# Kernel optimization log

Measured on AMD Instinct MI355X. Metric: run time of the kernel, lower is better.

The kernel has to match this reference:

```python
import jax, jax.numpy as jnp
import numpy as np

N = 100000      # nodes
R = 4           # relations
E = 500000      # edges per relation
IN, HID, OUT = 128, 128, 64


def _rel_conv(x, src, dst, W, b):
    """One DGL GraphConv (norm='both') over one relation's edge list.
    out = D_dst^{-1/2} * segsum_dst( D_src^{-1/2} x[src] ) @ W + b
    """
    ones = jnp.ones(src.shape[0], dtype=x.dtype)
    out_deg = jax.ops.segment_sum(ones, src, num_segments=N)
    in_deg = jax.ops.segment_sum(ones, dst, num_segments=N)
    norm_src = jax.lax.rsqrt(jnp.maximum(out_deg, 1.0))
    norm_dst = jax.lax.rsqrt(jnp.maximum(in_deg, 1.0))
    msg = (x * norm_src[:, None])[src]                       # [E, d] gather
    agg = jax.ops.segment_sum(msg, dst, num_segments=N)      # [N, d] scatter-add
    agg = agg * norm_dst[:, None]
    return agg @ W + b


def setup_inputs() -> dict:
    key = jax.random.key(0)
    ks = jax.random.split(key, 8)
    x = jax.random.normal(ks[0], (N, IN), dtype=jnp.float32)
    edge_src = jax.random.randint(ks[1], (R, E), 0, N, dtype=jnp.int32)
    edge_dst = jax.random.randint(ks[2], (R, E), 0, N, dtype=jnp.int32)
    s1 = 1.0 / np.sqrt(IN)
    s2 = 1.0 / np.sqrt(HID)
    W1 = jax.random.normal(ks[3], (R, IN, HID), dtype=jnp.float32) * s1
    b1 = jnp.zeros((R, HID), dtype=jnp.float32)
    W2 = jax.random.normal(ks[4], (R, HID, OUT), dtype=jnp.float32) * s2
    b2 = jnp.zeros((R, OUT), dtype=jnp.float32)
    return {"x": x, "edge_src": edge_src, "edge_dst": edge_dst,
            "W1": W1, "b1": b1, "W2": W2, "b2": b2}


def reference(x, edge_src, edge_dst, W1, b1, W2, b2):
    # layer 1: per-relation GraphConv, aggregate='sum' across relations
    h = _rel_conv(x, edge_src[0], edge_dst[0], W1[0], b1[0])
    for r in range(1, R):
        h = h + _rel_conv(x, edge_src[r], edge_dst[r], W1[r], b1[r])
    h = jax.nn.relu(h)
    # layer 2
    out = _rel_conv(h, edge_src[0], edge_dst[0], W2[0], b2[0])
    for r in range(1, R):
        out = out + _rel_conv(h, edge_src[r], edge_dst[r], W2[r], b2[r])
    return out
```

## Files before the change

kernel.cpp:

```cpp
#include <hip/hip_runtime.h>


constexpr int Nn  = 100000;
constexpr int Rr  = 4;
constexpr int Ee  = 500000;
constexpr int RE  = Rr * Ee;
constexpr int TOT = Rr * Nn;
constexpr int NP  = 100096;
constexpr int NPB = NP / 128;
constexpr int NB1 = 1024;
constexpr int CH  = (TOT + NB1 - 1) / NB1;

constexpr int CB2   = (RE / 2 + 255) / 256;
constexpr int GB1   = 4 * NPB;
constexpr int PAIR1 = 2 * GB1;
constexpr int P1_GRID = PAIR1 + (CB2 - GB1) + 1;

constexpr int FB = (RE / 4 + 255) / 256;

typedef short bf16x8 __attribute__((ext_vector_type(8)));
typedef float f32x4  __attribute__((ext_vector_type(4)));

__device__ __forceinline__ unsigned short f2bf(float f) {
    unsigned u = __builtin_bit_cast(unsigned, f);
    u = u + 0x7FFFu + ((u >> 16) & 1u);
    return (unsigned short)(u >> 16);
}
__device__ __forceinline__ float bf2f(unsigned short h) {
    unsigned u = ((unsigned)h) << 16;
    return __builtin_bit_cast(float, u);
}
__device__ __forceinline__ float bfbits_lo(unsigned p) {
    return __builtin_bit_cast(float, p << 16);
}
__device__ __forceinline__ float bfbits_hi(unsigned p) {
    return __builtin_bit_cast(float, p & 0xFFFF0000u);
}

__device__ __forceinline__ void count_body2(int sub, int tid,
    const int* __restrict__ src, const int* __restrict__ dst,
    unsigned* __restrict__ deg, unsigned* __restrict__ slot)
{
    int e0 = (sub * 256 + tid) * 2;
    if (e0 >= RE) return;
    int r = (unsigned)e0 / (unsigned)Ee;
    int base = r * Nn;
    int2 s2 = *reinterpret_cast<const int2*>(src + e0);
    int2 d2 = *reinterpret_cast<const int2*>(dst + e0);
    atomicAdd(&deg[base + s2.x], 1u);
    atomicAdd(&deg[base + s2.y], 1u);
    uint2 sl;
    sl.x = atomicAdd(&deg[TOT + d2.x * Rr + r], 1u);
    sl.y = atomicAdd(&deg[TOT + d2.y * Rr + r], 1u);
    *reinterpret_cast<uint2*>(slot + e0) = sl;
}

__device__ __forceinline__ void bsum_body(int tid,
    const float* __restrict__ b1, const float* __restrict__ b2,
    float* __restrict__ bs1, float* __restrict__ bs2)
{
    if (tid < 128) bs1[tid] = b1[tid] + b1[128 + tid] + b1[256 + tid] + b1[384 + tid];
    if (tid < 64)  bs2[tid] = b2[tid] + b2[64 + tid] + b2[128 + tid] + b2[192 + tid];
}

template<int BN, bool CONVA>
__device__ __forceinline__ void gemm_body(
    const short* __restrict__ Xh, const short* __restrict__ Xl,
    const float* __restrict__ Xf,
    const short* __restrict__ WhT_, const short* __restrict__ WlT_,
    short* __restrict__ Y_, int CW, int rowblk, int rel)
{
    constexpr int BM = 128, BKp = 40;
    constexpr int MFR = (BN == 128) ? 4 : 2;
    constexpr int NFR = 4;
    const short* WhT = WhT_ + (size_t)rel * (BN * 128);
    const short* WlT = WlT_ + (size_t)rel * (BN * 128);
    short* Y = Y_ + (size_t)rel * BN;

    __shared__ __align__(16) short Ah[BM * BKp], Al[BM * BKp];
    __shared__ __align__(16) short Bh[BN * BKp], Bl[BN * BKp];

    const int tid = threadIdx.x;
    const int lane = tid & 63, wid = tid >> 6;
    const int lr = lane & 15, lg = lane >> 4;
    const int wm0 = (BN == 128) ? (wid >> 1) * 64 : wid * 32;
    const int wn0 = (BN == 128) ? (wid & 1) * 64 : 0;
    const int row0 = rowblk * BM;

    f32x4 acc[MFR][NFR];
    #pragma unroll
    for (int m = 0; m < MFR; ++m)
        #pragma unroll
        for (int n = 0; n < NFR; ++n)
            #pragma unroll
            for (int j = 0; j < 4; ++j) acc[m][n][j] = 0.f;

    const int sr = tid >> 1;
    const int sko = (tid & 1) * 16;

    for (int ks = 0; ks < 4; ++ks) {
        if constexpr (CONVA) {
            int grow = row0 + sr;
            float v[16];
            if (grow < Nn) {
                const float* xp = Xf + (size_t)grow * 128 + ks * 32 + sko;
                float4 a0 = *reinterpret_cast<const float4*>(xp);
                float4 a1 = *reinterpret_cast<const float4*>(xp + 4);
                float4 a2 = *reinterpret_cast<const float4*>(xp + 8);
                float4 a3 = *reinterpret_cast<const float4*>(xp + 12);
                v[0]=a0.x; v[1]=a0.y; v[2]=a0.z; v[3]=a0.w;
                v[4]=a1.x; v[5]=a1.y; v[6]=a1.z; v[7]=a1.w;
                v[8]=a2.x; v[9]=a2.y; v[10]=a2.z; v[11]=a2.w;
                v[12]=a3.x; v[13]=a3.y; v[14]=a3.z; v[15]=a3.w;
            } else {
                #pragma unroll
                for (int i = 0; i < 16; ++i) v[i] = 0.f;
            }
            bf16x8 h0, h1, l0, l1;
            #pragma unroll
            for (int i = 0; i < 8; ++i) {
                unsigned short h = f2bf(v[i]);
                h0[i] = (short)h; l0[i] = (short)f2bf(v[i] - bf2f(h));
                unsigned short g = f2bf(v[8 + i]);
                h1[i] = (short)g; l1[i] = (short)f2bf(v[8 + i] - bf2f(g));
            }
            *reinterpret_cast<bf16x8*>(&Ah[sr * BKp + sko])     = h0;
            *reinterpret_cast<bf16x8*>(&Ah[sr * BKp + sko + 8]) = h1;
            *reinterpret_cast<bf16x8*>(&Al[sr * BKp + sko])     = l0;
            *reinterpret_cast<bf16x8*>(&Al[sr * BKp + sko + 8]) = l1;
        } else {
            size_t ga = (size_t)(row0 + sr) * 128 + ks * 32 + sko;
            *reinterpret_cast<bf16x8*>(&Ah[sr * BKp + sko])     = *reinterpret_cast<const bf16x8*>(&Xh[ga]);
            *reinterpret_cast<bf16x8*>(&Ah[sr * BKp + sko + 8]) = *reinterpret_cast<const bf16x8*>(&Xh[ga + 8]);
            *reinterpret_cast<bf16x8*>(&Al[sr * BKp + sko])     = *reinterpret_cast<const bf16x8*>(&Xl[ga]);
            *reinterpret_cast<bf16x8*>(&Al[sr * BKp + sko + 8]) = *reinterpret_cast<const bf16x8*>(&Xl[ga + 8]);
        }
        if (BN == 128 || tid < 128) {
            size_t gb = (size_t)sr * 128 + ks * 32 + sko;
            *reinterpret_cast<bf16x8*>(&Bh[sr * BKp + sko])     = *reinterpret_cast<const bf16x8*>(&WhT[gb]);
            *reinterpret_cast<bf16x8*>(&Bh[sr * BKp + sko + 8]) = *reinterpret_cast<const bf16x8*>(&WhT[gb + 8]);
            *reinterpret_cast<bf16x8*>(&Bl[sr * BKp + sko])     = *reinterpret_cast<const bf16x8*>(&WlT[gb]);
            *reinterpret_cast<bf16x8*>(&Bl[sr * BKp + sko + 8]) = *reinterpret_cast<const bf16x8*>(&WlT[gb + 8]);
        }
        __syncthreads();

        bf16x8 bh[NFR], bl[NFR];
        #pragma unroll
        for (int n = 0; n < NFR; ++n) {
            bh[n] = *reinterpret_cast<const bf16x8*>(&Bh[(wn0 + n * 16 + lr) * BKp + lg * 8]);
            bl[n] = *reinterpret_cast<const bf16x8*>(&Bl[(wn0 + n * 16 + lr) * BKp + lg * 8]);
        }
        __builtin_amdgcn_s_setprio(1);
        #pragma unroll
        for (int m = 0; m < MFR; ++m) {
            bf16x8 ah = *reinterpret_cast<const bf16x8*>(&Ah[(wm0 + m * 16 + lr) * BKp + lg * 8]);
            bf16x8 al = *reinterpret_cast<const bf16x8*>(&Al[(wm0 + m * 16 + lr) * BKp + lg * 8]);
            #pragma unroll
            for (int n = 0; n < NFR; ++n) {
                acc[m][n] = __builtin_amdgcn_mfma_f32_16x16x32_bf16(ah, bh[n], acc[m][n], 0, 0, 0);
                acc[m][n] = __builtin_amdgcn_mfma_f32_16x16x32_bf16(ah, bl[n], acc[m][n], 0, 0, 0);
                acc[m][n] = __builtin_amdgcn_mfma_f32_16x16x32_bf16(al, bh[n], acc[m][n], 0, 0, 0);
            }
        }
        __builtin_amdgcn_s_setprio(0);
        __syncthreads();
    }

    #pragma unroll
    for (int m = 0; m < MFR; ++m)
        #pragma unroll
        for (int n = 0; n < NFR; ++n) {
            int col = wn0 + n * 16 + lr;
            int rb = row0 + wm0 + m * 16 + lg * 4;
            #pragma unroll
            for (int j = 0; j < 4; ++j)
                Y[(size_t)(rb + j) * CW + col] = (short)f2bf(acc[m][n][j]);
        }
}

__global__ __launch_bounds__(256)
void phase1_kernel(const int* __restrict__ src, const int* __restrict__ dst,
                   unsigned* __restrict__ deg, unsigned* __restrict__ slot,
                   const float* __restrict__ X,
                   const short* __restrict__ w1h, const short* __restrict__ w1l,
                   short* __restrict__ Y,
                   const float* __restrict__ b1, const float* __restrict__ b2,
                   float* __restrict__ bs1, float* __restrict__ bs2)
{
    int bid = blockIdx.x, tid = threadIdx.x;
    if (bid < PAIR1) {
        int sub = bid >> 1;
        if (bid & 1) {
            int rel = sub & 3, rowblk = sub >> 2;
            gemm_body<128, true>(nullptr, nullptr, X, w1h, w1l, Y, 512, rowblk, rel);
        } else {
            count_body2(sub, tid, src, dst, deg, slot);
        }
    } else {
        int t = bid - PAIR1;
        if (t < CB2 - GB1) count_body2(GB1 + t, tid, src, dst, deg, slot);
        else              bsum_body(tid, b1, b2, bs1, bs2);
    }
}

__global__ __launch_bounds__(256)
void count_kernel(const int* __restrict__ src, const int* __restrict__ dst,
                  unsigned* __restrict__ deg, unsigned* __restrict__ slot)
{
    count_body2(blockIdx.x, threadIdx.x, src, dst, deg, slot);
}

__global__ void bsum_kernel(const float* __restrict__ b1, const float* __restrict__ b2,
                            float* __restrict__ bs1, float* __restrict__ bs2)
{
    bsum_body(threadIdx.x, b1, b2, bs1, bs2);
}

__global__ __launch_bounds__(256)
void norms_scan1_kernel(const unsigned* __restrict__ deg, float* __restrict__ nrm,
                        uint2* __restrict__ rpnd, unsigned* __restrict__ partial)
{
    __shared__ unsigned s[256];
    int b = blockIdx.x, t = threadIdx.x;
    int start = b * CH;
    int n = TOT - start; if (n > CH) n = CH;
    unsigned sum = 0;
    for (int i = t; i < n; i += 256) {
        unsigned sd = deg[start + i];
        unsigned dd = deg[TOT + start + i];
        nrm[start + i] = rsqrtf((float)(sd > 0u ? sd : 1u));
        rpnd[start + i].y = __builtin_bit_cast(unsigned, rsqrtf((float)(dd > 0u ? dd : 1u)));
        sum += dd;
    }
    s[t] = sum; __syncthreads();
    for (int d = 128; d > 0; d >>= 1) {
        if (t < d) s[t] += s[t + d];
        __syncthreads();
    }
    if (t == 0) partial[b] = s[0];
}

__global__ __launch_bounds__(1024)
void scan2_kernel(unsigned* __restrict__ partial, unsigned* __restrict__ rowptr)
{
    __shared__ unsigned s[NB1];
    int t = threadIdx.x;
    unsigned orig = partial[t];
    s[t] = orig; __syncthreads();
    for (int d = 1; d < NB1; d <<= 1) {
        unsigned v = (t >= d) ? s[t - d] : 0u;
        __syncthreads();
        s[t] += v;
        __syncthreads();
    }
    partial[t] = s[t] - orig;
    if (t == 0) rowptr[TOT] = (unsigned)RE;
}

__global__ __launch_bounds__(256)
void scan3_kernel(const unsigned* __restrict__ deg, const unsigned* __restrict__ base,
                  unsigned* __restrict__ rowptr, uint2* __restrict__ rpnd)
{
    __shared__ unsigned s[CH];
    int b = blockIdx.x, t = threadIdx.x;
    int start = b * CH;
    int n = TOT - start; if (n > CH) n = CH;
    if (n <= 0) return;
    for (int i = t; i < n; i += 256) s[i] = deg[TOT + start + i];
    __syncthreads();
    if (t == 0) {
        unsigned run = base[b];
        for (int i = 0; i < n; ++i) { unsigned v = s[i]; s[i] = run; run += v; }
    }
    __syncthreads();
    for (int i = t; i < n; i += 256) {
        unsigned v = s[i];
        rowptr[start + i] = v;
        rpnd[start + i].x = v;
    }
}

__global__ __launch_bounds__(256)
void fill_csr_kernel(const int* __restrict__ src, const int* __restrict__ dst,
                     const unsigned* __restrict__ slot, const uint2* __restrict__ rpnd,
                     const float* __restrict__ nrm, int2* __restrict__ csrw)
{
    int e0 = (blockIdx.x * 256 + threadIdx.x) * 4;
    if (e0 >= RE) return;
    int r = (unsigned)e0 / (unsigned)Ee;
    int base = r * Nn;
    int4 s4 = *reinterpret_cast<const int4*>(src + e0);
    int4 d4 = *reinterpret_cast<const int4*>(dst + e0);
    uint4 sl = *reinterpret_cast<const uint4*>(slot + e0);
    #pragma unroll
    for (int i = 0; i < 4; ++i) {
        int s = (i == 0) ? s4.x : (i == 1) ? s4.y : (i == 2) ? s4.z : s4.w;
        int d = (i == 0) ? d4.x : (i == 1) ? d4.y : (i == 2) ? d4.z : d4.w;
        unsigned k = (i == 0) ? sl.x : (i == 1) ? sl.y : (i == 2) ? sl.z : sl.w;
        uint2 rn = rpnd[d * Rr + r];
        float w = nrm[base + s] * __builtin_bit_cast(float, rn.y);
        int2 v; v.x = s | (r << 17); v.y = __builtin_bit_cast(int, w);
        csrw[rn.x + k] = v;
    }
}

__global__ __launch_bounds__(256)
void convw_kernel(const float* __restrict__ W1, const float* __restrict__ W2,
                  short* __restrict__ w1h, short* __restrict__ w1l,
                  short* __restrict__ w2h, short* __restrict__ w2l)
{
    int gid = blockIdx.x * 256 + threadIdx.x;
    if (gid < 4 * 128 * 128) {
        int r = gid >> 14, rem = gid & 16383, n = rem >> 7, k = rem & 127;
        float v = W1[(r << 14) + k * 128 + n];
        unsigned short h = f2bf(v);
        unsigned short l = f2bf(v - bf2f(h));
        w1h[(r << 14) + n * 128 + k] = (short)h;
        w1l[(r << 14) + n * 128 + k] = (short)l;
    } else {
        int g2 = gid - 65536;
        if (g2 >= 4 * 64 * 128) return;
        int r = g2 >> 13, rem = g2 & 8191, n = rem >> 7, k = rem & 127;
        float v = W2[(r << 13) + k * 64 + n];
        unsigned short h = f2bf(v);
        unsigned short l = f2bf(v - bf2f(h));
        w2h[(r << 13) + n * 128 + k] = (short)h;
        w2l[(r << 13) + n * 128 + k] = (short)l;
    }
}

template<int BN, bool CONVA>
__global__ __launch_bounds__(256)
void gemm_kernel(const short* __restrict__ Xh, const short* __restrict__ Xl,
                 const float* __restrict__ Xf,
                 const short* __restrict__ WhT_, const short* __restrict__ WlT_,
                 short* __restrict__ Y_, int CW)
{
    gemm_body<BN, CONVA>(Xh, Xl, Xf, WhT_, WlT_, Y_, CW, blockIdx.x, blockIdx.y);
}

template<int F, int NRl>
__global__ __launch_bounds__(256)
void gather_kernel(const short* __restrict__ Y, const unsigned* __restrict__ rowptr,
                   const int2* __restrict__ csrw, const float* __restrict__ bsum,
                   float* __restrict__ H, short* __restrict__ Xh, short* __restrict__ Xl,
                   int CW, int rel, int accumulate, int finalize)
{
    constexpr int FL = F / 16;
    int wid = (blockIdx.x * 256 + threadIdx.x) >> 6;
    int lane = threadIdx.x & 63;
    int q = lane >> 4, li = lane & 15;
    if (wid >= Nn) return;

    unsigned e, e1;
    if (NRl == 4) { e = rowptr[wid * 4];       e1 = rowptr[wid * 4 + 4]; }
    else          { e = rowptr[wid * 4 + rel]; e1 = rowptr[wid * 4 + rel + 1]; }

    float t[FL];
    #pragma unroll
    for (int f = 0; f < FL; ++f) t[f] = 0.f;

    auto yaddr = [&](int2 a) -> const short* {
        int s = a.x & 0x1FFFF;
        int rl = (NRl == 4) ? (a.x >> 17) : 0;
        return Y + (size_t)s * CW + rl * F + li * FL;
    };

    for (; e + 8 <= e1; e += 8) {
        int2 a = csrw[e + q], b = csrw[e + 4 + q];
        const short* ya = yaddr(a);
        const short* yb = yaddr(b);
        float wa = __builtin_bit_cast(float, a.y);
        float wb = __builtin_bit_cast(float, b.y);
        if constexpr (FL == 8) {
            uint4 pa = *reinterpret_cast<const uint4*>(ya);
            uint4 pb = *reinterpret_cast<const uint4*>(yb);
            t[0] += wa * bfbits_lo(pa.x) + wb * bfbits_lo(pb.x);
            t[1] += wa * bfbits_hi(pa.x) + wb * bfbits_hi(pb.x);
            t[2] += wa * bfbits_lo(pa.y) + wb * bfbits_lo(pb.y);
            t[3] += wa * bfbits_hi(pa.y) + wb * bfbits_hi(pb.y);
            t[4] += wa * bfbits_lo(pa.z) + wb * bfbits_lo(pb.z);
            t[5] += wa * bfbits_hi(pa.z) + wb * bfbits_hi(pb.z);
            t[6] += wa * bfbits_lo(pa.w) + wb * bfbits_lo(pb.w);
            t[7] += wa * bfbits_hi(pa.w) + wb * bfbits_hi(pb.w);
        } else {
            uint2 pa = *reinterpret_cast<const uint2*>(ya);
            uint2 pb = *reinterpret_cast<const uint2*>(yb);
            t[0] += wa * bfbits_lo(pa.x) + wb * bfbits_lo(pb.x);
            t[1] += wa * bfbits_hi(pa.x) + wb * bfbits_hi(pb.x);
            t[2] += wa * bfbits_lo(pa.y) + wb * bfbits_lo(pb.y);
            t[3] += wa * bfbits_hi(pa.y) + wb * bfbits_hi(pb.y);
        }
    }
    if (e + 4 <= e1) {
        int2 a = csrw[e + q];
        const short* ya = yaddr(a);
        float wa = __builtin_bit_cast(float, a.y);
        if constexpr (FL == 8) {
            uint4 pa = *reinterpret_cast<const uint4*>(ya);
            t[0] += wa * bfbits_lo(pa.x); t[1] += wa * bfbits_hi(pa.x);
            t[2] += wa * bfbits_lo(pa.y); t[3] += wa * bfbits_hi(pa.y);
            t[4] += wa * bfbits_lo(pa.z); t[5] += wa * bfbits_hi(pa.z);
            t[6] += wa * bfbits_lo(pa.w); t[7] += wa * bfbits_hi(pa.w);
        } else {
            uint2 pa = *reinterpret_cast<const uint2*>(ya);
            t[0] += wa * bfbits_lo(pa.x); t[1] += wa * bfbits_hi(pa.x);
            t[2] += wa * bfbits_lo(pa.y); t[3] += wa * bfbits_hi(pa.y);
        }
        e += 4;
    }
    int nrem = (int)(e1 - e);
    if (q < nrem) {
        int2 a = csrw[e + q];
        const short* ya = yaddr(a);
        float wa = __builtin_bit_cast(float, a.y);
        if constexpr (FL == 8) {
            uint4 pa = *reinterpret_cast<const uint4*>(ya);
            t[0] += wa * bfbits_lo(pa.x); t[1] += wa * bfbits_hi(pa.x);
            t[2] += wa * bfbits_lo(pa.y); t[3] += wa * bfbits_hi(pa.y);
            t[4] += wa * bfbits_lo(pa.z); t[5] += wa * bfbits_hi(pa.z);
            t[6] += wa * bfbits_lo(pa.w); t[7] += wa * bfbits_hi(pa.w);
        } else {
            uint2 pa = *reinterpret_cast<const uint2*>(ya);
            t[0] += wa * bfbits_lo(pa.x); t[1] += wa * bfbits_hi(pa.x);
            t[2] += wa * bfbits_lo(pa.y); t[3] += wa * bfbits_hi(pa.y);
        }
    }

    #pragma unroll
    for (int f = 0; f < FL; ++f) {
        t[f] += __shfl_xor(t[f], 16, 64);
        t[f] += __shfl_xor(t[f], 32, 64);
    }
    if (q != 0) return;

    float* hp = H + (size_t)wid * F + li * FL;
    if (accumulate) {
        #pragma unroll
        for (int f = 0; f < FL; ++f) t[f] += hp[f];
    } else {
        #pragma unroll
        for (int f = 0; f < FL; ++f) t[f] += bsum[li * FL + f];
    }
    if (F == 128 && finalize) {
        short hv[8], lv[8];
        #pragma unroll
        for (int f = 0; f < FL; ++f) {
            float v = fmaxf(t[f], 0.f);
            unsigned short hb = f2bf(v);
            hv[f] = (short)hb;
            lv[f] = (short)f2bf(v - bf2f(hb));
        }
        *reinterpret_cast<uint4*>(Xh + (size_t)wid * F + li * FL) = *reinterpret_cast<uint4*>(hv);
        *reinterpret_cast<uint4*>(Xl + (size_t)wid * F + li * FL) = *reinterpret_cast<uint4*>(lv);
    } else {
        if constexpr (FL == 8) {
            *reinterpret_cast<float4*>(hp)     = make_float4(t[0], t[1], t[2], t[3]);
            *reinterpret_cast<float4*>(hp + 4) = make_float4(t[4], t[5], t[6], t[7]);
        } else {
            *reinterpret_cast<float4*>(hp) = make_float4(t[0], t[1], t[2], t[3]);
        }
    }
}

extern "C" void kernel_launch(void* const* d_in, const int* in_sizes, int n_in,
                              void* d_out, int out_size, void* d_ws, size_t ws_size,
                              hipStream_t stream)
{
    const float* x  = (const float*)d_in[0];
    const int* esrc = (const int*)d_in[1];
    const int* edst = (const int*)d_in[2];
    const float* W1 = (const float*)d_in[3];
    const float* b1 = (const float*)d_in[4];
    const float* W2 = (const float*)d_in[5];
    const float* b2 = (const float*)d_in[6];
    float* out = (float*)d_out;

    char* ws = (char*)d_ws;
    size_t off = 0;
    auto alloc = [&](size_t bytes) { char* p = ws + off; off += (bytes + 255) & ~(size_t)255; return p; };
    unsigned* deg     = (unsigned*)alloc((size_t)2 * TOT * 4);
    float*    nrm     = (float*)   alloc((size_t)TOT * 4);
    uint2*    rpnd    = (uint2*)   alloc((size_t)TOT * 8);
    unsigned* rowptr  = (unsigned*)alloc((size_t)(TOT + 1) * 4);
    unsigned* partial = (unsigned*)alloc((size_t)NB1 * 4);
    unsigned* slot    = (unsigned*)alloc((size_t)RE * 4);
    float*    bs1     = (float*)   alloc(128 * 4);
    float*    bs2     = (float*)   alloc(64 * 4);
    short*    w1h     = (short*)   alloc((size_t)4 * 128 * 128 * 2);
    short*    w1l     = (short*)   alloc((size_t)4 * 128 * 128 * 2);
    short*    w2h     = (short*)   alloc((size_t)4 * 64 * 128 * 2);
    short*    w2l     = (short*)   alloc((size_t)4 * 64 * 128 * 2);
    int2*     csrw    = (int2*)    alloc((size_t)RE * 8);
    short*    xh      = (short*)   alloc((size_t)NP * 128 * 2);
    short*    xl      = (short*)   alloc((size_t)NP * 128 * 2);

    size_t yslot = (size_t)NP * 128 * 2;
    bool pathA = (ws_size >= off + 4 * yslot + 4096);
    float* h = nullptr;
    short* Y;
    if (pathA) {
        Y = (short*)alloc(4 * yslot);
    } else {
        h = (float*)alloc((size_t)NP * 128 * 4);
        Y = (short*)alloc(yslot);
    }

    const int ggrid = (Nn * 64 + 255) / 256;

    convw_kernel<<<384, 256, 0, stream>>>(W1, W2, w1h, w1l, w2h, w2l);
    hipMemsetAsync(deg, 0, (size_t)2 * TOT * 4, stream);

    if (pathA) {
        phase1_kernel<<<P1_GRID, 256, 0, stream>>>(
            esrc, edst, deg, slot, x, w1h, w1l, Y, b1, b2, bs1, bs2);
        norms_scan1_kernel<<<NB1, 256, 0, stream>>>(deg, nrm, rpnd, partial);
        scan2_kernel<<<1, NB1, 0, stream>>>(partial, rowptr);
        scan3_kernel<<<NB1, 256, 0, stream>>>(deg, partial, rowptr, rpnd);
        fill_csr_kernel<<<FB, 256, 0, stream>>>(esrc, edst, slot, rpnd, nrm, csrw);
        gather_kernel<128, 4><<<ggrid, 256, 0, stream>>>(
            Y, rowptr, csrw, bs1, (float*)out , xh, xl, 512, 0, 0, 1);
        gemm_kernel<64, false><<<dim3(NPB, 4), 256, 0, stream>>>(
            xh, xl, nullptr, w2h, w2l, Y, 256);
        gather_kernel<64, 4><<<ggrid, 256, 0, stream>>>(
            Y, rowptr, csrw, bs2, out, nullptr, nullptr, 256, 0, 0, 0);
    } else {
        count_kernel<<<CB2, 256, 0, stream>>>(esrc, edst, deg, slot);
        bsum_kernel<<<1, 128, 0, stream>>>(b1, b2, bs1, bs2);
        norms_scan1_kernel<<<NB1, 256, 0, stream>>>(deg, nrm, rpnd, partial);
        scan2_kernel<<<1, NB1, 0, stream>>>(partial, rowptr);
        scan3_kernel<<<NB1, 256, 0, stream>>>(deg, partial, rowptr, rpnd);
        fill_csr_kernel<<<FB, 256, 0, stream>>>(esrc, edst, slot, rpnd, nrm, csrw);
        for (int r = 0; r < Rr; ++r) {
            gemm_kernel<128, true><<<dim3(NPB, 1), 256, 0, stream>>>(
                nullptr, nullptr, x, w1h + (size_t)r * 128 * 128, w1l + (size_t)r * 128 * 128, Y, 128);
            gather_kernel<128, 1><<<ggrid, 256, 0, stream>>>(
                Y, rowptr, csrw, bs1, h, xh, xl, 128, r, r > 0, r == Rr - 1);
        }
        for (int r = 0; r < Rr; ++r) {
            gemm_kernel<64, false><<<dim3(NPB, 1), 256, 0, stream>>>(
                xh, xl, nullptr, w2h + (size_t)r * 64 * 128, w2l + (size_t)r * 64 * 128, Y, 64);
            gather_kernel<64, 1><<<ggrid, 256, 0, stream>>>(
                Y, rowptr, csrw, bs2, out, nullptr, nullptr, 64, r, r > 0, 0);
        }
    }
}
```

Baseline: 433.9 us.

## Fuse layer-2 GEMM across relations and widen gather unrolling

Adds a 512-thread GEMM kernel that computes all four relations' layer-2 projections in one block per 128-row tile. The A tile is loaded into shared memory once and reused across relations, instead of being reloaded by a separate grid dimension per relation. The gather kernel now unrolls four edges per quarter-wave. For F=64 it uses 8 lanes per edge with 16-byte loads instead of 16 lanes with 8-byte loads, so more edges are in flight per wave. The cost is a longer shuffle reduction and more registers and shared memory per block.

Result: faster. 396.6 us (-8.6%).

```diff
diff --git a/kernel.cpp b/kernel.cpp
--- a/kernel.cpp
+++ b/kernel.cpp
@@ -339,6 +339,77 @@
     gemm_body<BN, CONVA>(Xh, Xl, Xf, WhT_, WlT_, Y_, CW, blockIdx.x, blockIdx.y);
 }
 
+__global__ __launch_bounds__(512)
+void gemm64f_kernel(const short* __restrict__ Xh, const short* __restrict__ Xl,
+                    const short* __restrict__ w2h, const short* __restrict__ w2l,
+                    short* __restrict__ Y)
+{
+    constexpr int BKp = 40;
+    __shared__ __align__(16) short Ah[128 * BKp], Al[128 * BKp];
+    __shared__ __align__(16) short Bh[256 * BKp], Bl[256 * BKp];
+
+    const int tid = threadIdx.x;
+    const int lane = tid & 63, wv = tid >> 6;
+    const int rel = wv >> 1, wm0 = (wv & 1) * 64;
+    const int lr = lane & 15, lg = lane >> 4;
+    const int row0 = blockIdx.x * 128;
+
+    f32x4 acc[4][4];
+    #pragma unroll
+    for (int m = 0; m < 4; ++m)
+        #pragma unroll
+        for (int n = 0; n < 4; ++n)
+            #pragma unroll
+            for (int j = 0; j < 4; ++j) acc[m][n][j] = 0.f;
+
+    const int sra = tid >> 2, ska = (tid & 3) * 8;
+    const int rb = tid >> 7, nb = (tid >> 1) & 63, skb = (tid & 1) * 16;
+
+    for (int ks = 0; ks < 4; ++ks) {
+        size_t ga = (size_t)(row0 + sra) * 128 + ks * 32 + ska;
+        *reinterpret_cast<bf16x8*>(&Ah[sra * BKp + ska]) = *reinterpret_cast<const bf16x8*>(&Xh[ga]);
+        *reinterpret_cast<bf16x8*>(&Al[sra * BKp + ska]) = *reinterpret_cast<const bf16x8*>(&Xl[ga]);
+        size_t gb = (size_t)rb * (64 * 128) + (size_t)nb * 128 + ks * 32 + skb;
+        *reinterpret_cast<bf16x8*>(&Bh[(rb * 64 + nb) * BKp + skb])     = *reinterpret_cast<const bf16x8*>(&w2h[gb]);
+        *reinterpret_cast<bf16x8*>(&Bh[(rb * 64 + nb) * BKp + skb + 8]) = *reinterpret_cast<const bf16x8*>(&w2h[gb + 8]);
+        *reinterpret_cast<bf16x8*>(&Bl[(rb * 64 + nb) * BKp + skb])     = *reinterpret_cast<const bf16x8*>(&w2l[gb]);
+        *reinterpret_cast<bf16x8*>(&Bl[(rb * 64 + nb) * BKp + skb + 8]) = *reinterpret_cast<const bf16x8*>(&w2l[gb + 8]);
+        __syncthreads();
+
+        bf16x8 bh[4], bl[4];
+        #pragma unroll
+        for (int n = 0; n < 4; ++n) {
+            bh[n] = *reinterpret_cast<const bf16x8*>(&Bh[(rel * 64 + n * 16 + lr) * BKp + lg * 8]);
+            bl[n] = *reinterpret_cast<const bf16x8*>(&Bl[(rel * 64 + n * 16 + lr) * BKp + lg * 8]);
+        }
+        __builtin_amdgcn_s_setprio(1);
+        #pragma unroll
+        for (int m = 0; m < 4; ++m) {
+            bf16x8 ah = *reinterpret_cast<const bf16x8*>(&Ah[(wm0 + m * 16 + lr) * BKp + lg * 8]);
+            bf16x8 al = *reinterpret_cast<const bf16x8*>(&Al[(wm0 + m * 16 + lr) * BKp + lg * 8]);
+            #pragma unroll
+            for (int n = 0; n < 4; ++n) {
+                acc[m][n] = __builtin_amdgcn_mfma_f32_16x16x32_bf16(ah, bh[n], acc[m][n], 0, 0, 0);
+                acc[m][n] = __builtin_amdgcn_mfma_f32_16x16x32_bf16(ah, bl[n], acc[m][n], 0, 0, 0);
+                acc[m][n] = __builtin_amdgcn_mfma_f32_16x16x32_bf16(al, bh[n], acc[m][n], 0, 0, 0);
+            }
+        }
+        __builtin_amdgcn_s_setprio(0);
+        __syncthreads();
+    }
+
+    #pragma unroll
+    for (int m = 0; m < 4; ++m)
+        #pragma unroll
+        for (int n = 0; n < 4; ++n) {
+            int col = rel * 64 + n * 16 + lr;
+            int rbse = row0 + wm0 + m * 16 + lg * 4;
+            #pragma unroll
+            for (int j = 0; j < 4; ++j)
+                Y[(size_t)(rbse + j) * 256 + col] = (short)f2bf(acc[m][n][j]);
+        }
+}
+
 template<int F, int NRl>
 __global__ __launch_bounds__(256)
 void gather_kernel(const short* __restrict__ Y, const unsigned* __restrict__ rowptr,
@@ -346,10 +417,12 @@
                    float* __restrict__ H, short* __restrict__ Xh, short* __restrict__ Xl,
                    int CW, int rel, int accumulate, int finalize)
 {
-    constexpr int FL = F / 16;
+    constexpr int LPE = (F == 128) ? 16 : 8;
+    constexpr int QN  = 64 / LPE;
+    constexpr int FL  = F / LPE;
     int wid = (blockIdx.x * 256 + threadIdx.x) >> 6;
     int lane = threadIdx.x & 63;
-    int q = lane >> 4, li = lane & 15;
+    int q = lane / LPE, li = lane & (LPE - 1);
     if (wid >= Nn) return;
 
     unsigned e, e1;
@@ -365,72 +438,64 @@
         int rl = (NRl == 4) ? (a.x >> 17) : 0;
         return Y + (size_t)s * CW + rl * F + li * FL;
     };
-
-    for (; e + 8 <= e1; e += 8) {
-        int2 a = csrw[e + q], b = csrw[e + 4 + q];
-        const short* ya = yaddr(a);
-        const short* yb = yaddr(b);
-        float wa = __builtin_bit_cast(float, a.y);
-        float wb = __builtin_bit_cast(float, b.y);
-        if constexpr (FL == 8) {
-            uint4 pa = *reinterpret_cast<const uint4*>(ya);
-            uint4 pb = *reinterpret_cast<const uint4*>(yb);
-            t[0] += wa * bfbits_lo(pa.x) + wb * bfbits_lo(pb.x);
-            t[1] += wa * bfbits_hi(pa.x) + wb * bfbits_hi(pb.x);
-            t[2] += wa * bfbits_lo(pa.y) + wb * bfbits_lo(pb.y);
-            t[3] += wa * bfbits_hi(pa.y) + wb * bfbits_hi(pb.y);
-            t[4] += wa * bfbits_lo(pa.z) + wb * bfbits_lo(pb.z);
-            t[5] += wa * bfbits_hi(pa.z) + wb * bfbits_hi(pb.z);
-            t[6] += wa * bfbits_lo(pa.w) + wb * bfbits_lo(pb.w);
-            t[7] += wa * bfbits_hi(pa.w) + wb * bfbits_hi(pb.w);
-        } else {
-            uint2 pa = *reinterpret_cast<const uint2*>(ya);
-            uint2 pb = *reinterpret_cast<const uint2*>(yb);
-            t[0] += wa * bfbits_lo(pa.x) + wb * bfbits_lo(pb.x);
-            t[1] += wa * bfbits_hi(pa.x) + wb * bfbits_hi(pb.x);
-            t[2] += wa * bfbits_lo(pa.y) + wb * bfbits_lo(pb.y);
-            t[3] += wa * bfbits_hi(pa.y) + wb * bfbits_hi(pb.y);
-        }
-    }
-    if (e + 4 <= e1) {
-        int2 a = csrw[e + q];
+    auto accum1 = [&](int2 a) {
         const short* ya = yaddr(a);
         float wa = __builtin_bit_cast(float, a.y);
-        if constexpr (FL == 8) {
-            uint4 pa = *reinterpret_cast<const uint4*>(ya);
-            t[0] += wa * bfbits_lo(pa.x); t[1] += wa * bfbits_hi(pa.x);
-            t[2] += wa * bfbits_lo(pa.y); t[3] += wa * bfbits_hi(pa.y);
-            t[4] += wa * bfbits_lo(pa.z); t[5] += wa * bfbits_hi(pa.z);
-            t[6] += wa * bfbits_lo(pa.w); t[7] += wa * bfbits_hi(pa.w);
-        } else {
-            uint2 pa = *reinterpret_cast<const uint2*>(ya);
-            t[0] += wa * bfbits_lo(pa.x); t[1] += wa * bfbits_hi(pa.x);
-            t[2] += wa * bfbits_lo(pa.y); t[3] += wa * bfbits_hi(pa.y);
-        }
-        e += 4;
+        uint4 pa = *reinterpret_cast<const uint4*>(ya);
+        t[0] += wa * bfbits_lo(pa.x); t[1] += wa * bfbits_hi(pa.x);
+        t[2] += wa * bfbits_lo(pa.y); t[3] += wa * bfbits_hi(pa.y);
+        t[4] += wa * bfbits_lo(pa.z); t[5] += wa * bfbits_hi(pa.z);
+        t[6] += wa * bfbits_lo(pa.w); t[7] += wa * bfbits_hi(pa.w);
+    };
+
+    for (; e + 4 * QN <= e1; e += 4 * QN) {
+        int2 a0 = csrw[e + q], a1 = csrw[e + QN + q];
+        int2 a2 = csrw[e + 2 * QN + q], a3 = csrw[e + 3 * QN + q];
+        const short* y0 = yaddr(a0); const short* y1 = yaddr(a1);
+        const short* y2 = yaddr(a2); const short* y3 = yaddr(a3);
+        float w0 = __builtin_bit_cast(float, a0.y), w1 = __builtin_bit_cast(float, a1.y);
+        float w2 = __builtin_bit_cast(float, a2.y), w3 = __builtin_bit_cast(float, a3.y);
+        uint4 p0 = *reinterpret_cast<const uint4*>(y0);
+        uint4 p1 = *reinterpret_cast<const uint4*>(y1);
+        uint4 p2 = *reinterpret_cast<const uint4*>(y2);
+        uint4 p3 = *reinterpret_cast<const uint4*>(y3);
+        t[0] += w0*bfbits_lo(p0.x) + w1*bfbits_lo(p1.x) + w2*bfbits_lo(p2.x) + w3*bfbits_lo(p3.x);
+        t[1] += w0*bfbits_hi(p0.x) + w1*bfbits_hi(p1.x) + w2*bfbits_hi(p2.x) + w3*bfbits_hi(p3.x);
+        t[2] += w0*bfbits_lo(p0.y) + w1*bfbits_lo(p1.y) + w2*bfbits_lo(p2.y) + w3*bfbits_lo(p3.y);
+        t[3] += w0*bfbits_hi(p0.y) + w1*bfbits_hi(p1.y) + w2*bfbits_hi(p2.y) + w3*bfbits_hi(p3.y);
+        t[4] += w0*bfbits_lo(p0.z) + w1*bfbits_lo(p1.z) + w2*bfbits_lo(p2.z) + w3*bfbits_lo(p3.z);
+        t[5] += w0*bfbits_hi(p0.z) + w1*bfbits_hi(p1.z) + w2*bfbits_hi(p2.z) + w3*bfbits_hi(p3.z);
+        t[6] += w0*bfbits_lo(p0.w) + w1*bfbits_lo(p1.w) + w2*bfbits_lo(p2.w) + w3*bfbits_lo(p3.w);
+        t[7] += w0*bfbits_hi(p0.w) + w1*bfbits_hi(p1.w) + w2*bfbits_hi(p2.w) + w3*bfbits_hi(p3.w);
+    }
+    if (e + 2 * QN <= e1) {
+        int2 a0 = csrw[e + q], a1 = csrw[e + QN + q];
+        const short* y0 = yaddr(a0); const short* y1 = yaddr(a1);
+        float w0 = __builtin_bit_cast(float, a0.y), w1 = __builtin_bit_cast(float, a1.y);
+        uint4 p0 = *reinterpret_cast<const uint4*>(y0);
+        uint4 p1 = *reinterpret_cast<const uint4*>(y1);
+        t[0] += w0*bfbits_lo(p0.x) + w1*bfbits_lo(p1.x);
+        t[1] += w0*bfbits_hi(p0.x) + w1*bfbits_hi(p1.x);
+        t[2] += w0*bfbits_lo(p0.y) + w1*bfbits_lo(p1.y);
+        t[3] += w0*bfbits_hi(p0.y) + w1*bfbits_hi(p1.y);
+        t[4] += w0*bfbits_lo(p0.z) + w1*bfbits_lo(p1.z);
+        t[5] += w0*bfbits_hi(p0.z) + w1*bfbits_hi(p1.z);
+        t[6] += w0*bfbits_lo(p0.w) + w1*bfbits_lo(p1.w);
+        t[7] += w0*bfbits_hi(p0.w) + w1*bfbits_hi(p1.w);
+        e += 2 * QN;
+    }
+    if (e + QN <= e1) {
+        accum1(csrw[e + q]);
+        e += QN;
     }
     int nrem = (int)(e1 - e);
-    if (q < nrem) {
-        int2 a = csrw[e + q];
-        const short* ya = yaddr(a);
-        float wa = __builtin_bit_cast(float, a.y);
-        if constexpr (FL == 8) {
-            uint4 pa = *reinterpret_cast<const uint4*>(ya);
-            t[0] += wa * bfbits_lo(pa.x); t[1] += wa * bfbits_hi(pa.x);
-            t[2] += wa * bfbits_lo(pa.y); t[3] += wa * bfbits_hi(pa.y);
-            t[4] += wa * bfbits_lo(pa.z); t[5] += wa * bfbits_hi(pa.z);
-            t[6] += wa * bfbits_lo(pa.w); t[7] += wa * bfbits_hi(pa.w);
-        } else {
-            uint2 pa = *reinterpret_cast<const uint2*>(ya);
-            t[0] += wa * bfbits_lo(pa.x); t[1] += wa * bfbits_hi(pa.x);
-            t[2] += wa * bfbits_lo(pa.y); t[3] += wa * bfbits_hi(pa.y);
-        }
-    }
+    if (q < nrem) accum1(csrw[e + q]);
 
     #pragma unroll
     for (int f = 0; f < FL; ++f) {
-        t[f] += __shfl_xor(t[f], 16, 64);
-        t[f] += __shfl_xor(t[f], 32, 64);
+        #pragma unroll
+        for (int o = LPE; o < 64; o <<= 1)
+            t[f] += __shfl_xor(t[f], o, 64);
     }
     if (q != 0) return;
 
@@ -454,12 +519,8 @@
         *reinterpret_cast<uint4*>(Xh + (size_t)wid * F + li * FL) = *reinterpret_cast<uint4*>(hv);
         *reinterpret_cast<uint4*>(Xl + (size_t)wid * F + li * FL) = *reinterpret_cast<uint4*>(lv);
     } else {
-        if constexpr (FL == 8) {
-            *reinterpret_cast<float4*>(hp)     = make_float4(t[0], t[1], t[2], t[3]);
-            *reinterpret_cast<float4*>(hp + 4) = make_float4(t[4], t[5], t[6], t[7]);
-        } else {
-            *reinterpret_cast<float4*>(hp) = make_float4(t[0], t[1], t[2], t[3]);
-        }
+        *reinterpret_cast<float4*>(hp)     = make_float4(t[0], t[1], t[2], t[3]);
+        *reinterpret_cast<float4*>(hp + 4) = make_float4(t[4], t[5], t[6], t[7]);
     }
 }
 
@@ -520,8 +581,7 @@
         fill_csr_kernel<<<FB, 256, 0, stream>>>(esrc, edst, slot, rpnd, nrm, csrw);
         gather_kernel<128, 4><<<ggrid, 256, 0, stream>>>(
             Y, rowptr, csrw, bs1, (float*)out , xh, xl, 512, 0, 0, 1);
-        gemm_kernel<64, false><<<dim3(NPB, 4), 256, 0, stream>>>(
-            xh, xl, nullptr, w2h, w2l, Y, 256);
+        gemm64f_kernel<<<NPB, 512, 0, stream>>>(xh, xl, w2h, w2l, Y);
         gather_kernel<64, 4><<<ggrid, 256, 0, stream>>>(
             Y, rowptr, csrw, bs2, out, nullptr, nullptr, 256, 0, 0, 0);
     } else {
```
